# Optimization experiments

Hardware: AMD Instinct MI355X
Metric: run time of the kernel (lower is better)

The kernel has to match this reference:

```python
import jax, jax.numpy as jnp
import numpy as np

NUM_CLASSES = 1000
FEAT_DIM = 128
BATCH = 2048
ALPHA = 1.0


def setup_inputs() -> dict:
    key = jax.random.key(0)
    k1, k2, k3 = jax.random.split(key, 3)
    feat = jax.random.normal(k1, (BATCH, FEAT_DIM), dtype=jnp.float32)
    label = jax.random.randint(k2, (BATCH,), 0, NUM_CLASSES, dtype=jnp.int64)
    # centers ~ kaiming_uniform_(a=sqrt(5)) on a (C, D) matrix -> U(-b, b), b = sqrt(6/((1+5)*D)) = 1/sqrt(D)
    bound = 1.0 / np.sqrt(FEAT_DIM)
    centers = jax.random.uniform(k3, (NUM_CLASSES, FEAT_DIM), dtype=jnp.float32,
                                 minval=-bound, maxval=bound)
    return {"feat": feat, "label": label, "centers": centers}


def reference(feat, label, centers):
    # feat: [B, D], centers: [C, D], label: [B]
    batch_size = feat.shape[0]
    # squared euclidean distance to every center: [B, C]
    diff = feat[:, None, :] - centers[None, :, :]          # [B, C, D]
    dist = jnp.sum(diff * diff, axis=-1)                   # [B, C]
    # margin scaling: multiply true-class distance by (1 + alpha)
    y_onehot = jax.nn.one_hot(label, centers.shape[0], dtype=dist.dtype) * ALPHA + 1.0
    margin_dist = dist * y_onehot
    margin_logits = -0.5 * margin_dist
    logits = -0.5 * dist
    # likelihood regularizer: mean of half squared distance to own center
    cdiff = feat - centers[label]                          # [B, D]
    likelihood = (1.0 / batch_size) * jnp.sum(cdiff * cdiff) / 2.0
    return logits, margin_logits, likelihood
```

## Files before the change

kernel.cpp:

```cpp
#include <hip/hip_runtime.h>
#include <hip/hip_bf16.h>

#define BATCH 2048
#define NCLS  1000
#define FEAT  128

typedef short bf16x8 __attribute__((ext_vector_type(8)));
typedef float f32x16 __attribute__((ext_vector_type(16)));

#define WS_LP   0
#define WS_FN   512
#define WS_CN   2560
#define WS_FB   4096
#define WS_CB   135168

__device__ inline unsigned int f2bf(float f) {
    unsigned int u;
    __builtin_memcpy(&u, &f, 4);
    return (u + 0x7fffu + ((u >> 16) & 1u)) >> 16;
}

__global__ __launch_bounds__(256) void prep_kernel(
    const float* __restrict__ feat,
    const float* __restrict__ centers,
    const int* __restrict__ label,
    float* __restrict__ ws)
{
    __shared__ float lp[4];
    int w    = blockIdx.x * 4 + (threadIdx.x >> 6);
    int lane = threadIdx.x & 63;
    float* fn = ws + WS_FN;
    float* cn = ws + WS_CN;
    unsigned int* fb = (unsigned int*)(ws + WS_FB);
    unsigned int* cb = (unsigned int*)(ws + WS_CB);

    if (w < BATCH) {
        int b = w;
        float2 f = *(const float2*)(feat + b * FEAT + lane * 2);
        int lb = label[b];
        float2 c = *(const float2*)(centers + lb * FEAT + lane * 2);
        fb[b * 64 + lane] = f2bf(f.x) | (f2bf(f.y) << 16);
        float fs = f.x * f.x + f.y * f.y;
        float d0 = f.x - c.x, d1 = f.y - c.y;
        float ls = d0 * d0 + d1 * d1;
        #pragma unroll
        for (int off = 32; off > 0; off >>= 1) {
            fs += __shfl_down(fs, off, 64);
            ls += __shfl_down(ls, off, 64);
        }
        if (lane == 0) {
            fn[b] = fs;
            lp[threadIdx.x >> 6] = ls;
        }
    } else if (w < BATCH + NCLS) {
        int c = w - BATCH;
        float2 cv = *(const float2*)(centers + c * FEAT + lane * 2);
        cb[c * 64 + lane] = f2bf(cv.x) | (f2bf(cv.y) << 16);
        float cs = cv.x * cv.x + cv.y * cv.y;
        #pragma unroll
        for (int off = 32; off > 0; off >>= 1) cs += __shfl_down(cs, off, 64);
        if (lane == 0) cn[c] = cs;
    }

    if (blockIdx.x < 512) {
        __syncthreads();
        if (threadIdx.x == 0)
            ws[WS_LP + blockIdx.x] = lp[0] + lp[1] + lp[2] + lp[3];
    }
}

__global__ __launch_bounds__(256) void lgm_main_kernel(
    const int* __restrict__ label,
    const float* __restrict__ ws,
    float* __restrict__ out)
{
    const float* fn = ws + WS_FN;
    const float* cn = ws + WS_CN;
    const unsigned short* fb = (const unsigned short*)(ws + WS_FB);
    const unsigned short* cb = (const unsigned short*)(ws + WS_CB);

    int tid     = threadIdx.x;
    int lane    = tid & 63;
    int wave    = tid >> 6;
    int tileCol = blockIdx.x & 15;
    int tileRow = blockIdx.x >> 4;
    int rowBase = tileRow * 64 + (wave & 1) * 32;
    int colBase = tileCol * 64 + (wave >> 1) * 32;
    int m       = lane & 31;
    int half    = lane >> 5;

    int r  = rowBase + m;
    int c0 = colBase + m;
    int c  = (c0 < NCLS) ? c0 : (NCLS - 1);

    const unsigned short* ap = fb + r * FEAT + half * 8;
    const unsigned short* bp = cb + c * FEAT + half * 8;

    f32x16 acc = {};
    #pragma unroll
    for (int kk = 0; kk < 8; kk++) {
        bf16x8 a = *(const bf16x8*)(ap + kk * 16);
        bf16x8 b = *(const bf16x8*)(bp + kk * 16);
        acc = __builtin_amdgcn_mfma_f32_32x32x16_bf16(a, b, acc, 0, 0, 0);
    }

    float* out0 = out;
    float* out1 = out + BATCH * NCLS;
    float cnv = cn[c];
    bool  colOK = (c0 < NCLS);
    #pragma unroll
    for (int reg = 0; reg < 16; reg++) {
        int row = rowBase + (reg & 3) + 8 * (reg >> 2) + 4 * half;
        if (colOK) {
            float dist  = fn[row] + cnv - 2.0f * acc[reg];
            float logit = -0.5f * dist;
            int idx = row * NCLS + c0;
            out0[idx] = logit;
            out1[idx] = (c0 == label[row]) ? 2.0f * logit : logit;
        }
    }

    if (blockIdx.x == 0 && tid < 64) {
        float s = 0.0f;
        #pragma unroll
        for (int j = 0; j < 8; j++) s += ws[WS_LP + lane + 64 * j];
        #pragma unroll
        for (int off = 32; off > 0; off >>= 1) s += __shfl_down(s, off, 64);
        if (lane == 0) out[2 * BATCH * NCLS] = s * (0.5f / (float)BATCH);
    }
}

extern "C" void kernel_launch(void* const* d_in, const int* in_sizes, int n_in,
                              void* d_out, int out_size, void* d_ws, size_t ws_size,
                              hipStream_t stream) {
    const float* feat    = (const float*)d_in[0];
    const int*   label   = (const int*)d_in[1];
    const float* centers = (const float*)d_in[2];
    float* ws = (float*)d_ws;

    prep_kernel<<<762, 256, 0, stream>>>(feat, centers, label, ws);
    lgm_main_kernel<<<512, 256, 0, stream>>>(label, ws, (float*)d_out);
}
```

Measured before the change: 72.13 us.

## Fuse bf16 conversion and norms into the MFMA kernel, derive likelihood from distances

```diff
diff --git a/kernel.cpp b/kernel.cpp
--- a/kernel.cpp
+++ b/kernel.cpp
@@ -1,5 +1,4 @@
 #include <hip/hip_runtime.h>
-#include <hip/hip_bf16.h>
 
 #define BATCH 2048
 #define NCLS  1000
@@ -8,76 +7,34 @@
 typedef short bf16x8 __attribute__((ext_vector_type(8)));
 typedef float f32x16 __attribute__((ext_vector_type(16)));
 
-#define WS_LP   0
-#define WS_FN   512
-#define WS_CN   2560
-#define WS_FB   4096
-#define WS_CB   135168
-
-__device__ inline unsigned int f2bf(float f) {
+__device__ __forceinline__ unsigned int f2bf(float f) {
     unsigned int u;
     __builtin_memcpy(&u, &f, 4);
     return (u + 0x7fffu + ((u >> 16) & 1u)) >> 16;
 }
 
-__global__ __launch_bounds__(256) void prep_kernel(
+__device__ __forceinline__ bf16x8 cvt_chunk(const float* __restrict__ p, float& nrm) {
+    float4 lo = *(const float4*)p;
+    float4 hi = *(const float4*)(p + 4);
+    nrm += lo.x * lo.x + lo.y * lo.y + lo.z * lo.z + lo.w * lo.w +
+           hi.x * hi.x + hi.y * hi.y + hi.z * hi.z + hi.w * hi.w;
+    bf16x8 r;
+    r[0] = (short)f2bf(lo.x); r[1] = (short)f2bf(lo.y);
+    r[2] = (short)f2bf(lo.z); r[3] = (short)f2bf(lo.w);
+    r[4] = (short)f2bf(hi.x); r[5] = (short)f2bf(hi.y);
+    r[6] = (short)f2bf(hi.z); r[7] = (short)f2bf(hi.w);
+    return r;
+}
+
+__global__ __launch_bounds__(256) void lgm_fused(
     const float* __restrict__ feat,
     const float* __restrict__ centers,
     const int* __restrict__ label,
-    float* __restrict__ ws)
-{
-    __shared__ float lp[4];
-    int w    = blockIdx.x * 4 + (threadIdx.x >> 6);
-    int lane = threadIdx.x & 63;
-    float* fn = ws + WS_FN;
-    float* cn = ws + WS_CN;
-    unsigned int* fb = (unsigned int*)(ws + WS_FB);
-    unsigned int* cb = (unsigned int*)(ws + WS_CB);
-
-    if (w < BATCH) {
-        int b = w;
-        float2 f = *(const float2*)(feat + b * FEAT + lane * 2);
-        int lb = label[b];
-        float2 c = *(const float2*)(centers + lb * FEAT + lane * 2);
-        fb[b * 64 + lane] = f2bf(f.x) | (f2bf(f.y) << 16);
-        float fs = f.x * f.x + f.y * f.y;
-        float d0 = f.x - c.x, d1 = f.y - c.y;
-        float ls = d0 * d0 + d1 * d1;
-        #pragma unroll
-        for (int off = 32; off > 0; off >>= 1) {
-            fs += __shfl_down(fs, off, 64);
-            ls += __shfl_down(ls, off, 64);
-        }
-        if (lane == 0) {
-            fn[b] = fs;
-            lp[threadIdx.x >> 6] = ls;
-        }
-    } else if (w < BATCH + NCLS) {
-        int c = w - BATCH;
-        float2 cv = *(const float2*)(centers + c * FEAT + lane * 2);
-        cb[c * 64 + lane] = f2bf(cv.x) | (f2bf(cv.y) << 16);
-        float cs = cv.x * cv.x + cv.y * cv.y;
-        #pragma unroll
-        for (int off = 32; off > 0; off >>= 1) cs += __shfl_down(cs, off, 64);
-        if (lane == 0) cn[c] = cs;
-    }
-
-    if (blockIdx.x < 512) {
-        __syncthreads();
-        if (threadIdx.x == 0)
-            ws[WS_LP + blockIdx.x] = lp[0] + lp[1] + lp[2] + lp[3];
-    }
-}
-
-__global__ __launch_bounds__(256) void lgm_main_kernel(
-    const int* __restrict__ label,
-    const float* __restrict__ ws,
+    float* __restrict__ ws,
     float* __restrict__ out)
 {
-    const float* fn = ws + WS_FN;
-    const float* cn = ws + WS_CN;
-    const unsigned short* fb = (const unsigned short*)(ws + WS_FB);
-    const unsigned short* cb = (const unsigned short*)(ws + WS_CB);
+    __shared__ float fn_lds[64];
+    __shared__ float red[4];
 
     int tid     = threadIdx.x;
     int lane    = tid & 63;
@@ -93,41 +50,62 @@
     int c0 = colBase + m;
     int c  = (c0 < NCLS) ? c0 : (NCLS - 1);
 
-    const unsigned short* ap = fb + r * FEAT + half * 8;
-    const unsigned short* bp = cb + c * FEAT + half * 8;
+    const float* ap = feat    + r * FEAT + half * 8;
+    const float* bp = centers + c * FEAT + half * 8;
 
+    float fs = 0.0f, cs = 0.0f;
     f32x16 acc = {};
     #pragma unroll
     for (int kk = 0; kk < 8; kk++) {
-        bf16x8 a = *(const bf16x8*)(ap + kk * 16);
-        bf16x8 b = *(const bf16x8*)(bp + kk * 16);
+        bf16x8 a = cvt_chunk(ap + kk * 16, fs);
+        bf16x8 b = cvt_chunk(bp + kk * 16, cs);
         acc = __builtin_amdgcn_mfma_f32_32x32x16_bf16(a, b, acc, 0, 0, 0);
     }
 
+    fs += __shfl_xor(fs, 32, 64);
+    cs += __shfl_xor(cs, 32, 64);
+    fn_lds[(wave & 1) * 32 + m] = fs;
+    __syncthreads();
+
     float* out0 = out;
     float* out1 = out + BATCH * NCLS;
-    float cnv = cn[c];
+    float cnv   = cs;
     bool  colOK = (c0 < NCLS);
+    int   rlb   = (wave & 1) * 32;
+    float lsum  = 0.0f;
     #pragma unroll
     for (int reg = 0; reg < 16; reg++) {
-        int row = rowBase + (reg & 3) + 8 * (reg >> 2) + 4 * half;
+        int rl  = rlb + (reg & 3) + 8 * (reg >> 2) + 4 * half;
+        int row = tileRow * 64 + rl;
         if (colOK) {
-            float dist  = fn[row] + cnv - 2.0f * acc[reg];
+            float dist  = fn_lds[rl] + cnv - 2.0f * acc[reg];
             float logit = -0.5f * dist;
-            int idx = row * NCLS + c0;
+            int   idx   = row * NCLS + c0;
+            bool  match = (c0 == label[row]);
             out0[idx] = logit;
-            out1[idx] = (c0 == label[row]) ? 2.0f * logit : logit;
+            out1[idx] = match ? 2.0f * logit : logit;
+            if (match) lsum += dist;
         }
     }
 
-    if (blockIdx.x == 0 && tid < 64) {
-        float s = 0.0f;
-        #pragma unroll
-        for (int j = 0; j < 8; j++) s += ws[WS_LP + lane + 64 * j];
-        #pragma unroll
-        for (int off = 32; off > 0; off >>= 1) s += __shfl_down(s, off, 64);
-        if (lane == 0) out[2 * BATCH * NCLS] = s * (0.5f / (float)BATCH);
-    }
+    #pragma unroll
+    for (int off = 32; off > 0; off >>= 1) lsum += __shfl_down(lsum, off, 64);
+    if (lane == 0) red[wave] = lsum;
+    __syncthreads();
+    if (tid == 0) ws[blockIdx.x] = red[0] + red[1] + red[2] + red[3];
+}
+
+__global__ __launch_bounds__(64) void lgm_finish(
+    const float* __restrict__ ws,
+    float* __restrict__ out)
+{
+    int lane = threadIdx.x;
+    float s = 0.0f;
+    #pragma unroll
+    for (int j = 0; j < 8; j++) s += ws[lane + 64 * j];
+    #pragma unroll
+    for (int off = 32; off > 0; off >>= 1) s += __shfl_down(s, off, 64);
+    if (lane == 0) out[2 * BATCH * NCLS] = s * (0.5f / (float)BATCH);
 }
 
 extern "C" void kernel_launch(void* const* d_in, const int* in_sizes, int n_in,
@@ -138,6 +116,6 @@
     const float* centers = (const float*)d_in[2];
     float* ws = (float*)d_ws;
 
-    prep_kernel<<<762, 256, 0, stream>>>(feat, centers, label, ws);
-    lgm_main_kernel<<<512, 256, 0, stream>>>(label, ws, (float*)d_out);
+    lgm_fused<<<512, 256, 0, stream>>>(feat, centers, label, ws, (float*)d_out);
+    lgm_finish<<<1, 64, 0, stream>>>(ws, (float*)d_out);
 }
```

Result: slower. 75.88 us (+5.2%).
